# Kernel tuning notes

Hardware: AMD Instinct MI355X
Metric: run time of the kernel (lower is better)

## Reference

```python
import jax, jax.numpy as jnp
import numpy as np

BATCH = 512          # bs_large + bs_small
COMBINED_BS = 320    # bs_large + bs_small // (r_large // r_small)
R = 64               # r_large
K = 4096             # hidden dim, fixed in the TIR kernel
N_ADAPT = 80         # combined adapters


def setup_inputs() -> dict:
    key = jax.random.key(0)
    k1, k2, k3, k4 = jax.random.split(key, 4)
    x = jax.random.normal(k1, (BATCH, 1, K), dtype=jnp.float32)
    xids = jax.random.randint(k2, (COMBINED_BS * R,), 0, BATCH, dtype=jnp.int32)
    wids = jax.random.randint(k3, (COMBINED_BS,), 0, N_ADAPT, dtype=jnp.int32)
    A = jax.random.normal(k4, (N_ADAPT, K, R), dtype=jnp.float32) * 0.02
    return {"x": x, "xids": xids, "wids": wids, "A": A}


def reference(x, xids, wids, A):
    # out[c, 0, r] = sum_k x[xids[c*R + r], 0, k] * A[wids[c], k, r]
    C = wids.shape[0]
    r = A.shape[2]
    tok = xids.reshape(C, r)          # per-output-element token ids
    xg = x[tok, 0, :]                 # (C, R, K) gathered activations
    Ag = A[wids]                      # (C, K, R) gathered adapters
    out = jnp.einsum('crk,ckr->cr', xg, Ag)
    return out[:, None, :]            # (C, 1, R)
```

## Files before the change

kernel.cpp:

```cpp
#include <hip/hip_runtime.h>

namespace {
constexpr int CBS   = 320;
constexpr int R     = 64;
constexpr int K     = 4096;
constexpr int SPLIT = 4;
constexpr int KS    = K / SPLIT;
constexpr int TK    = 64;
constexpr int NT    = 256;
constexpr int NW    = NT / 64;
constexpr int LSTRIDE = TK + 1;
}

__global__ __launch_bounds__(NT)
void lora_a_kernel(const float* __restrict__ x,
                   const int*   __restrict__ xids,
                   const int*   __restrict__ wids,
                   const float* __restrict__ A,
                   float*       __restrict__ out)
{
    __shared__ float xs[R * LSTRIDE];
    __shared__ float red[NW * R];

    const int bid  = blockIdx.x;
    const int c    = bid / SPLIT;
    const int s    = bid % SPLIT;
    const int t    = threadIdx.x;
    const int wave = t >> 6;
    const int lane = t & 63;

    const int wid = wids[c];
    const float* __restrict__ Aw = A + (size_t)wid * (K * R);

    const int rw  = t >> 2;
    const int jq  = t & 3;
    const int tok = xids[c * R + rw];
    const float* __restrict__ xrow = x + (size_t)tok * K + s * KS + jq * 16;

    float acc = 0.0f;

    for (int tile = 0; tile < KS / TK; ++tile) {
        const float4* __restrict__ src = (const float4*)(xrow + tile * TK);
        float* dst = xs + rw * LSTRIDE + jq * 16;
#pragma unroll
        for (int ii = 0; ii < 4; ++ii) {
            float4 v = src[ii];
            dst[ii * 4 + 0] = v.x;
            dst[ii * 4 + 1] = v.y;
            dst[ii * 4 + 2] = v.z;
            dst[ii * 4 + 3] = v.w;
        }
        __syncthreads();

        const int k0 = s * KS + tile * TK + wave * (TK / NW);
        const float* __restrict__ Ap = Aw + (size_t)k0 * R + lane;
        const float* __restrict__ xp = xs + lane * LSTRIDE + wave * (TK / NW);
#pragma unroll
        for (int i = 0; i < TK / NW; ++i) {
            acc = fmaf(xp[i], Ap[(size_t)i * R], acc);
        }
        __syncthreads();
    }

    red[wave * R + lane] = acc;
    __syncthreads();
    if (wave == 0) {
        float sum = red[lane] + red[R + lane] + red[2 * R + lane] + red[3 * R + lane];
        atomicAdd(&out[c * R + lane], sum);
    }
}

extern "C" void kernel_launch(void* const* d_in, const int* in_sizes, int n_in,
                              void* d_out, int out_size, void* d_ws, size_t ws_size,
                              hipStream_t stream)
{
    (void)in_sizes; (void)n_in; (void)d_ws; (void)ws_size;
    const float* x    = (const float*)d_in[0];
    const int*   xids = (const int*)d_in[1];
    const int*   wids = (const int*)d_in[2];
    const float* A    = (const float*)d_in[3];
    float* out        = (float*)d_out;

    hipMemsetAsync(out, 0, (size_t)out_size * sizeof(float), stream);

    hipLaunchKernelGGL(lora_a_kernel, dim3(CBS * SPLIT), dim3(NT), 0, stream,
                       x, xids, wids, A, out);
}
```

Before: 158.5 us.

## Double the K split, prefetch x into registers, vectorize A loads

The K split rises from 4 to 8, giving twice as many blocks. Each thread now prefetches the next x tile into registers while the current one is computed. The x tile is stored transposed in shared memory so each lane reads float4 of x and A across four r outputs, and the partial sums are combined with wave shuffles before the block reduction. This targets memory-bound load throughput and latency, at the cost of more atomics and possible LDS bank conflicts on the transposed stores.

```diff
diff --git a/kernel.cpp b/kernel.cpp
--- a/kernel.cpp
+++ b/kernel.cpp
@@ -4,12 +4,12 @@
 constexpr int CBS   = 320;
 constexpr int R     = 64;
 constexpr int K     = 4096;
-constexpr int SPLIT = 4;
+constexpr int SPLIT = 8;
 constexpr int KS    = K / SPLIT;
 constexpr int TK    = 64;
 constexpr int NT    = 256;
 constexpr int NW    = NT / 64;
-constexpr int LSTRIDE = TK + 1;
+constexpr int NTILES = KS / TK;
 }
 
 __global__ __launch_bounds__(NT)
@@ -19,15 +19,17 @@
                    const float* __restrict__ A,
                    float*       __restrict__ out)
 {
-    __shared__ float xs[R * LSTRIDE];
+    __shared__ float xs[TK * R];
     __shared__ float red[NW * R];
 
     const int bid  = blockIdx.x;
-    const int c    = bid / SPLIT;
-    const int s    = bid % SPLIT;
+    const int c    = bid >> 3;
+    const int s    = bid & 7;
     const int t    = threadIdx.x;
     const int wave = t >> 6;
     const int lane = t & 63;
+    const int r4   = lane & 15;
+    const int kq   = lane >> 4;
 
     const int wid = wids[c];
     const float* __restrict__ Aw = A + (size_t)wid * (K * R);
@@ -37,33 +39,60 @@
     const int tok = xids[c * R + rw];
     const float* __restrict__ xrow = x + (size_t)tok * K + s * KS + jq * 16;
 
-    float acc = 0.0f;
+    float4 acc = make_float4(0.f, 0.f, 0.f, 0.f);
 
-    for (int tile = 0; tile < KS / TK; ++tile) {
-        const float4* __restrict__ src = (const float4*)(xrow + tile * TK);
-        float* dst = xs + rw * LSTRIDE + jq * 16;
+    float4 pv[4];
+    {
+        const float4* src = (const float4*)xrow;
+#pragma unroll
+        for (int ii = 0; ii < 4; ++ii) pv[ii] = src[ii];
+    }
+
+    for (int tile = 0; tile < NTILES; ++tile) {
 #pragma unroll
         for (int ii = 0; ii < 4; ++ii) {
-            float4 v = src[ii];
-            dst[ii * 4 + 0] = v.x;
-            dst[ii * 4 + 1] = v.y;
-            dst[ii * 4 + 2] = v.z;
-            dst[ii * 4 + 3] = v.w;
+            const int kk = jq * 16 + ii * 4;
+            xs[(kk + 0) * R + rw] = pv[ii].x;
+            xs[(kk + 1) * R + rw] = pv[ii].y;
+            xs[(kk + 2) * R + rw] = pv[ii].z;
+            xs[(kk + 3) * R + rw] = pv[ii].w;
         }
         __syncthreads();
 
-        const int k0 = s * KS + tile * TK + wave * (TK / NW);
-        const float* __restrict__ Ap = Aw + (size_t)k0 * R + lane;
-        const float* __restrict__ xp = xs + lane * LSTRIDE + wave * (TK / NW);
+        if (tile + 1 < NTILES) {
+            const float4* src = (const float4*)(xrow + (tile + 1) * TK);
 #pragma unroll
-        for (int i = 0; i < TK / NW; ++i) {
-            acc = fmaf(xp[i], Ap[(size_t)i * R], acc);
+            for (int ii = 0; ii < 4; ++ii) pv[ii] = src[ii];
+        }
+
+        const int kw = wave * 16 + kq;
+        const float* __restrict__ Ap =
+            Aw + (size_t)(s * KS + tile * TK + kw) * R + 4 * r4;
+#pragma unroll
+        for (int i = 0; i < 4; ++i) {
+            float4 av = *(const float4*)(Ap + (size_t)(4 * i) * R);
+            float4 xv = *(const float4*)(&xs[(kw + 4 * i) * R + 4 * r4]);
+            acc.x = fmaf(xv.x, av.x, acc.x);
+            acc.y = fmaf(xv.y, av.y, acc.y);
+            acc.z = fmaf(xv.z, av.z, acc.z);
+            acc.w = fmaf(xv.w, av.w, acc.w);
         }
         __syncthreads();
     }
 
-    red[wave * R + lane] = acc;
+#pragma unroll
+    for (int m = 16; m < 64; m <<= 1) {
+        acc.x += __shfl_xor(acc.x, m, 64);
+        acc.y += __shfl_xor(acc.y, m, 64);
+        acc.z += __shfl_xor(acc.z, m, 64);
+        acc.w += __shfl_xor(acc.w, m, 64);
+    }
+    if (kq == 0) {
+        float* rd = &red[wave * R + 4 * r4];
+        rd[0] = acc.x; rd[1] = acc.y; rd[2] = acc.z; rd[3] = acc.w;
+    }
     __syncthreads();
+
     if (wave == 0) {
         float sum = red[lane] + red[R + lane] + red[2 * R + lane] + red[3 * R + lane];
         atomicAdd(&out[c * R + lane], sum);
```

Result: no change. 156.0 us (-1.6%).

## Group combined rows by adapter so each A slice load serves several rows

Applied to the files above, without the earlier changes.

Each block now builds an in-block histogram of adapter ids and assigns itself a group of up to four combined rows that share the same adapter. Each wave loads a K-slice of A into registers once and applies it to all rows in the group. Activations are read directly from global memory with float4 loads instead of being staged through shared memory, and K is split 32 ways. This cuts redundant A traffic, which dominates memory reads, at the price of every block redoing the histogram and rank computation over wids, an O(n^2) rank scan, and idle tail blocks when groups are not full.

```diff
diff --git a/kernel.cpp b/kernel.cpp
--- a/kernel.cpp
+++ b/kernel.cpp
@@ -1,73 +1,110 @@
 #include <hip/hip_runtime.h>
+#include <stdint.h>
 
 namespace {
-constexpr int CBS   = 320;
-constexpr int R     = 64;
-constexpr int K     = 4096;
-constexpr int SPLIT = 4;
-constexpr int KS    = K / SPLIT;
-constexpr int TK    = 64;
-constexpr int NT    = 256;
-constexpr int NW    = NT / 64;
-constexpr int LSTRIDE = TK + 1;
+constexpr int BATCH  = 512;
+constexpr int CBS    = 320;
+constexpr int R      = 64;
+constexpr int K      = 4096;
+constexpr int NADAPT = 80;
+constexpr int SPLIT  = 32;
+constexpr int KS     = K / SPLIT;
+constexpr int NBODY  = KS / 32;
+constexpr int G      = 4;
+constexpr int MAXG   = (CBS + (G - 1) * NADAPT) / G;
+constexpr int NT     = 256;
+constexpr int NBLK   = MAXG * SPLIT / (NT / 64);
 }
 
-__global__ __launch_bounds__(NT)
-void lora_a_kernel(const float* __restrict__ x,
-                   const int*   __restrict__ xids,
-                   const int*   __restrict__ wids,
-                   const float* __restrict__ A,
-                   float*       __restrict__ out)
+__global__ __launch_bounds__(NT, 4)
+void lora_main(const float* __restrict__ x,
+               const int*   __restrict__ xids,
+               const int*   __restrict__ wids,
+               const float* __restrict__ A,
+               float*       __restrict__ out)
 {
-    __shared__ float xs[R * LSTRIDE];
-    __shared__ float red[NW * R];
+    __shared__ int swids[CBS];
+    __shared__ int hist[NADAPT];
+    __shared__ int gmem[G];
+    __shared__ int meta[2];
 
-    const int bid  = blockIdx.x;
-    const int c    = bid / SPLIT;
-    const int s    = bid % SPLIT;
-    const int t    = threadIdx.x;
+    const int t      = threadIdx.x;
+    const int my_gid = blockIdx.x >> 3;
+
+    for (int i = t; i < CBS; i += NT) swids[i] = wids[i];
+    if (t < NADAPT) hist[t] = 0;
+    if (t == 0) meta[0] = -1;
+    __syncthreads();
+    for (int i = t; i < CBS; i += NT) atomicAdd(&hist[swids[i]], 1);
+    __syncthreads();
+    if (t == 0) {
+        int run = 0;
+        for (int w = 0; w < NADAPT; ++w) {
+            const int gb = run;
+            run += (hist[w] + G - 1) >> 2;
+            if (my_gid >= gb && my_gid < run) { meta[0] = w; meta[1] = (my_gid - gb) << 2; }
+        }
+    }
+    __syncthreads();
+    const int wid = meta[0];
+    if (wid < 0) return;
+    const int base_rank = meta[1];
+    const int cnt = min(G, hist[wid] - base_rank);
+    for (int i = t; i < CBS; i += NT) {
+        if (swids[i] == wid) {
+            int rk = 0;
+            for (int j = 0; j < i; ++j) rk += (swids[j] == wid) ? 1 : 0;
+            if (rk >= base_rank && rk < base_rank + G) gmem[rk - base_rank] = i;
+        }
+    }
+    __syncthreads();
+
     const int wave = t >> 6;
     const int lane = t & 63;
+    const int s    = ((blockIdx.x & 7) << 2) | wave;
 
-    const int wid = wids[c];
-    const float* __restrict__ Aw = A + (size_t)wid * (K * R);
+    const float* __restrict__ Ap =
+        A + (size_t)wid * (K * R) + (size_t)(s * KS) * R + lane;
 
-    const int rw  = t >> 2;
-    const int jq  = t & 3;
-    const int tok = xids[c * R + rw];
-    const float* __restrict__ xrow = x + (size_t)tok * K + s * KS + jq * 16;
-
-    float acc = 0.0f;
-
-    for (int tile = 0; tile < KS / TK; ++tile) {
-        const float4* __restrict__ src = (const float4*)(xrow + tile * TK);
-        float* dst = xs + rw * LSTRIDE + jq * 16;
+    int cidx[G];
+    const float4* __restrict__ xp[G];
 #pragma unroll
-        for (int ii = 0; ii < 4; ++ii) {
-            float4 v = src[ii];
-            dst[ii * 4 + 0] = v.x;
-            dst[ii * 4 + 1] = v.y;
-            dst[ii * 4 + 2] = v.z;
-            dst[ii * 4 + 3] = v.w;
-        }
-        __syncthreads();
-
-        const int k0 = s * KS + tile * TK + wave * (TK / NW);
-        const float* __restrict__ Ap = Aw + (size_t)k0 * R + lane;
-        const float* __restrict__ xp = xs + lane * LSTRIDE + wave * (TK / NW);
-#pragma unroll
-        for (int i = 0; i < TK / NW; ++i) {
-            acc = fmaf(xp[i], Ap[(size_t)i * R], acc);
-        }
-        __syncthreads();
+    for (int g = 0; g < G; ++g) {
+        cidx[g] = (g < cnt) ? gmem[g] : gmem[0];
+        const int tok = xids[cidx[g] * R + lane];
+        xp[g] = (const float4*)(x + (size_t)tok * K + s * KS);
     }
 
-    red[wave * R + lane] = acc;
-    __syncthreads();
-    if (wave == 0) {
-        float sum = red[lane] + red[R + lane] + red[2 * R + lane] + red[3 * R + lane];
-        atomicAdd(&out[c * R + lane], sum);
+    float acc[G] = {0.f, 0.f, 0.f, 0.f};
+
+#pragma unroll
+    for (int b = 0; b < NBODY; ++b) {
+        float a[32];
+#pragma unroll
+        for (int j = 0; j < 32; ++j)
+            a[j] = Ap[(size_t)(b * 32 + j) * R];
+
+#pragma unroll
+        for (int g = 0; g < G; ++g) {
+            if (g < cnt) {
+                float tacc = acc[g];
+#pragma unroll
+                for (int j = 0; j < 8; ++j) {
+                    const float4 v = xp[g][b * 8 + j];
+                    tacc = fmaf(v.x, a[j * 4 + 0], tacc);
+                    tacc = fmaf(v.y, a[j * 4 + 1], tacc);
+                    tacc = fmaf(v.z, a[j * 4 + 2], tacc);
+                    tacc = fmaf(v.w, a[j * 4 + 3], tacc);
+                }
+                acc[g] = tacc;
+            }
+        }
     }
+
+#pragma unroll
+    for (int g = 0; g < G; ++g)
+        if (g < cnt)
+            atomicAdd(&out[cidx[g] * R + lane], acc[g]);
 }
 
 extern "C" void kernel_launch(void* const* d_in, const int* in_sizes, int n_in,
@@ -83,6 +120,6 @@
 
     hipMemsetAsync(out, 0, (size_t)out_size * sizeof(float), stream);
 
-    hipLaunchKernelGGL(lora_a_kernel, dim3(CBS * SPLIT), dim3(NT), 0, stream,
+    hipLaunchKernelGGL(lora_main, dim3(NBLK), dim3(NT), 0, stream,
                        x, xids, wids, A, out);
 }
```

After: 184.2 us. 1.16x slower.
